# Kernel tuning notes

Hardware: AMD Instinct MI355X
Metric: run time of the kernel (lower is better)

The kernel has to match this reference:

```python
import jax, jax.numpy as jnp
import numpy as np

B, N, E, H = 16, 577, 1024, 16          # batch, tokens (1 cls + 24x24 patches), embed, heads
HD = E // H
LORA_E, LORA_R = 4, 16                   # LoRA experts, rank
AD_E, AD_D = 4, 64                       # adapter experts, bottleneck
FF = 4 * E


def setup_inputs() -> dict:
    key = jax.random.key(0)
    ks = jax.random.split(key, 12)
    p = lambda i, shape: jax.random.normal(ks[i], shape, dtype=jnp.float32) * 0.02
    return {
        "tokens": jax.random.normal(ks[0], (B, N, E), dtype=jnp.float32),
        "ln1_g": jnp.ones((E,), jnp.float32), "ln1_b": jnp.zeros((E,), jnp.float32),
        "qkv_w": p(1, (3 * E, E)), "qkv_b": jnp.zeros((3 * E,), jnp.float32),
        "proj_w": p(2, (E, E)), "proj_b": jnp.zeros((E,), jnp.float32),
        "lora_gate_w": p(3, (LORA_E, E)),
        "lora_A": p(4, (LORA_E, LORA_R, E)),
        "lora_B": p(5, (LORA_E, 3 * E, LORA_R)),
        "ln2_g": jnp.ones((E,), jnp.float32), "ln2_b": jnp.zeros((E,), jnp.float32),
        "fc1_w": p(6, (FF, E)), "fc1_b": jnp.zeros((FF,), jnp.float32),
        "fc2_w": p(7, (E, FF)), "fc2_b": jnp.zeros((E,), jnp.float32),
        "ad_gate_w": p(8, (AD_E, E)),
        "ad_down_w": p(9, (AD_E, AD_D, E)), "ad_down_b": jnp.zeros((AD_E, AD_D), jnp.float32),
        "ad_up_w": p(10, (AD_E, E, AD_D)), "ad_up_b": jnp.zeros((AD_E, E), jnp.float32),
    }


def _ln(x, g, b):
    m = x.mean(-1, keepdims=True)
    v = ((x - m) ** 2).mean(-1, keepdims=True)
    return (x - m) * jax.lax.rsqrt(v + 1e-6) * g + b


def reference(tokens, ln1_g, ln1_b, qkv_w, qkv_b, proj_w, proj_b,
              lora_gate_w, lora_A, lora_B, ln2_g, ln2_b,
              fc1_w, fc1_b, fc2_w, fc2_b,
              ad_gate_w, ad_down_w, ad_down_b, ad_up_w, ad_up_b):
    # ---- attention with MoE-LoRA delta on fused QKV ----
    normed = _ln(tokens, ln1_g, ln1_b)                      # [B,N,E]
    qkv = normed @ qkv_w.T + qkv_b                          # [B,N,3E]
    gates = jax.nn.softmax(normed @ lora_gate_w.T, axis=-1)  # [B,N,X]
    h = jnp.einsum('bnd,xrd->bnxr', normed, lora_A)         # low-rank down
    delta = jnp.einsum('bnxr,bnx,xor->bno', h, gates, lora_B)  # gate-weighted up
    qkv = (qkv + delta).reshape(B, N, 3, H, HD).transpose(2, 0, 3, 1, 4)
    q, k, v = qkv[0], qkv[1], qkv[2]                        # [B,H,N,hd]
    scores = jnp.einsum('bhqd,bhkd->bhqk', q, k) * (HD ** -0.5)
    probs = jax.nn.softmax(scores, axis=-1)
    ctx = jnp.einsum('bhqk,bhkd->bhqd', probs, v)
    ctx = ctx.transpose(0, 2, 1, 3).reshape(B, N, E)
    tokens = tokens + (ctx @ proj_w.T + proj_b)
    # ---- MLP + MoE adapter branch (shared norm2 input) ----
    mlp_in = _ln(tokens, ln2_g, ln2_b)
    mlp_out = jax.nn.gelu(mlp_in @ fc1_w.T + fc1_b, approximate=False) @ fc2_w.T + fc2_b
    ag = jax.nn.softmax(mlp_in @ ad_gate_w.T, axis=-1)       # [B,N,Xa]
    ah = jax.nn.gelu(jnp.einsum('bnd,xhd->bnxh', mlp_in, ad_down_w) + ad_down_b,
                     approximate=False)
    ad_out = (jnp.einsum('bnxh,bnx,xoh->bno', ah, ag, ad_up_w)
              + jnp.einsum('bnx,xo->bno', ag, ad_up_b))
    return tokens + mlp_out + ad_out
```

## Files before the change

### kernel.cpp

```cpp
#include <hip/hip_runtime.h>
#include <math.h>

#define TOK 9232
#define EMB 1024
#define NQKV 3072
#define FFD 4096
#define NSEQ 577

typedef __bf16 bf16x8 __attribute__((ext_vector_type(8)));
typedef float f32x4 __attribute__((ext_vector_type(4)));
typedef unsigned short ushort8 __attribute__((ext_vector_type(8)));
typedef unsigned short ushort4v __attribute__((ext_vector_type(4)));

typedef __attribute__((address_space(3))) unsigned int lds_u32_t;
typedef const __attribute__((address_space(1))) unsigned int glob_u32_t;

__device__ __forceinline__ void async16(void* lds, const void* g) {
    __builtin_amdgcn_global_load_lds((glob_u32_t*)g, (lds_u32_t*)lds, 16, 0, 0);
}

__device__ __forceinline__ unsigned short f2bf(float f) {
    unsigned int u = __builtin_bit_cast(unsigned int, f);
    u = (u + 0x7fffu + ((u >> 16) & 1u)) >> 16;
    return (unsigned short)u;
}
__device__ __forceinline__ float bf2f(unsigned short s) {
    unsigned int u = ((unsigned int)s) << 16;
    return __builtin_bit_cast(float, u);
}
__device__ __forceinline__ float gelu_exact(float x) {
    return 0.5f * x * (1.0f + erff(x * 0.70710678118654752f));
}

__global__ void k_pack_all(const float* __restrict__ s_qkv, const float* __restrict__ s_proj,
                           const float* __restrict__ s_fc1, const float* __restrict__ s_fc2,
                           const float* __restrict__ s_la,  const float* __restrict__ s_ad,
                           unsigned short* __restrict__ d_qkv, unsigned short* __restrict__ d_proj,
                           unsigned short* __restrict__ d_fc1, unsigned short* __restrict__ d_fc2,
                           unsigned short* __restrict__ d_la,  unsigned short* __restrict__ d_ad) {
    int stride = gridDim.x * 256;
    for (int i4 = blockIdx.x * 256 + threadIdx.x; i4 < 3227648; i4 += stride) {
        const float* s; unsigned short* d; int local;
        if (i4 < 786432)       { s = s_qkv;  d = d_qkv;  local = i4; }
        else if (i4 < 1048576) { s = s_proj; d = d_proj; local = i4 - 786432; }
        else if (i4 < 2097152) { s = s_fc1;  d = d_fc1;  local = i4 - 1048576; }
        else if (i4 < 3145728) { s = s_fc2;  d = d_fc2;  local = i4 - 2097152; }
        else if (i4 < 3162112) { s = s_la;   d = d_la;   local = i4 - 3145728; }
        else                   { s = s_ad;   d = d_ad;   local = i4 - 3162112; }
        float4 v = ((const float4*)s)[local];
        ushort4v o;
        o[0] = f2bf(v.x); o[1] = f2bf(v.y); o[2] = f2bf(v.z); o[3] = f2bf(v.w);
        ((ushort4v*)d)[local] = o;
    }
}
__global__ void k_pack_bcat(const float* __restrict__ Bw, unsigned short* __restrict__ out) {
    int i = blockIdx.x * 256 + threadIdx.x;
    if (i >= 3072 * 64) return;
    int o = i >> 6, j = i & 63, x = j >> 4, r = j & 15;
    out[o * 64 + j] = f2bf(Bw[x * 3072 * 16 + o * 16 + r]);
}
__global__ void k_pack_u(const float* __restrict__ Uw, unsigned short* __restrict__ out) {
    int i = blockIdx.x * 256 + threadIdx.x;
    if (i >= 1024 * 256) return;
    int o = i >> 8, j = i & 255, x = j >> 6, h = j & 63;
    out[o * 256 + j] = f2bf(Uw[x * 65536 + o * 64 + h]);
}

__global__ __launch_bounds__(256) void k_ln_gates(const float* __restrict__ x,
                                                  const float* __restrict__ g,
                                                  const float* __restrict__ b,
                                                  const float* __restrict__ gw,
                                                  unsigned short* __restrict__ out,
                                                  float* __restrict__ gates) {
    int t = blockIdx.x;
    int tid = threadIdx.x;
    const float* xp = x + (size_t)t * EMB;
    float4 v = ((const float4*)xp)[tid];
    float s = v.x + v.y + v.z + v.w;
    float sq = v.x * v.x + v.y * v.y + v.z * v.z + v.w * v.w;
    #pragma unroll
    for (int off = 32; off > 0; off >>= 1) {
        s += __shfl_down(s, off);
        sq += __shfl_down(sq, off);
    }
    __shared__ float red[8];
    if ((tid & 63) == 0) { red[tid >> 6] = s; red[(tid >> 6) + 4] = sq; }
    __syncthreads();
    float S = red[0] + red[1] + red[2] + red[3];
    float SQ = red[4] + red[5] + red[6] + red[7];
    float mean = S * (1.0f / EMB);
    float var = SQ * (1.0f / EMB) - mean * mean;
    float rstd = rsqrtf(var + 1e-6f);
    float4 gv = ((const float4*)g)[tid];
    float4 bv = ((const float4*)b)[tid];
    float n0 = (v.x - mean) * rstd * gv.x + bv.x;
    float n1 = (v.y - mean) * rstd * gv.y + bv.y;
    float n2 = (v.z - mean) * rstd * gv.z + bv.z;
    float n3 = (v.w - mean) * rstd * gv.w + bv.w;
    ushort4v o;
    o[0] = f2bf(n0); o[1] = f2bf(n1); o[2] = f2bf(n2); o[3] = f2bf(n3);
    ((ushort4v*)(out + (size_t)t * EMB))[tid] = o;
    float p[4];
    #pragma unroll
    for (int xx = 0; xx < 4; ++xx) {
        float4 gr = ((const float4*)(gw + xx * EMB))[tid];
        p[xx] = n0 * gr.x + n1 * gr.y + n2 * gr.z + n3 * gr.w;
    }
    #pragma unroll
    for (int off = 32; off > 0; off >>= 1) {
        #pragma unroll
        for (int xx = 0; xx < 4; ++xx) p[xx] += __shfl_down(p[xx], off);
    }
    __shared__ float red2[4][4];
    if ((tid & 63) == 0) {
        #pragma unroll
        for (int xx = 0; xx < 4; ++xx) red2[tid >> 6][xx] = p[xx];
    }
    __syncthreads();
    if (tid == 0) {
        float l[4];
        #pragma unroll
        for (int xx = 0; xx < 4; ++xx) l[xx] = red2[0][xx] + red2[1][xx] + red2[2][xx] + red2[3][xx];
        float m = fmaxf(fmaxf(l[0], l[1]), fmaxf(l[2], l[3]));
        float e[4], ssum = 0.f;
        #pragma unroll
        for (int xx = 0; xx < 4; ++xx) { e[xx] = expf(l[xx] - m); ssum += e[xx]; }
        float inv = 1.0f / ssum;
        #pragma unroll
        for (int xx = 0; xx < 4; ++xx) gates[t * 4 + xx] = e[xx] * inv;
    }
}

__global__ __launch_bounds__(256) void k_fc2init(const float* __restrict__ tok2,
                                                 const float* __restrict__ fc2b,
                                                 const float* __restrict__ ag,
                                                 const float* __restrict__ upb,
                                                 float* __restrict__ out) {
    int t = blockIdx.x;
    int tid = threadIdx.x;
    float g0 = ag[t * 4 + 0], g1 = ag[t * 4 + 1], g2 = ag[t * 4 + 2], g3 = ag[t * 4 + 3];
    float4 b0 = ((const float4*)(upb + 0 * EMB))[tid];
    float4 b1 = ((const float4*)(upb + 1 * EMB))[tid];
    float4 b2 = ((const float4*)(upb + 2 * EMB))[tid];
    float4 b3 = ((const float4*)(upb + 3 * EMB))[tid];
    float4 fb = ((const float4*)fc2b)[tid];
    float4 r = ((const float4*)(tok2 + (size_t)t * EMB))[tid];
    r.x += fb.x + g0 * b0.x + g1 * b1.x + g2 * b2.x + g3 * b3.x;
    r.y += fb.y + g0 * b0.y + g1 * b1.y + g2 * b2.y + g3 * b3.y;
    r.z += fb.z + g0 * b0.z + g1 * b1.z + g2 * b2.z + g3 * b3.z;
    r.w += fb.w + g0 * b0.w + g1 * b1.w + g2 * b2.w + g3 * b3.w;
    ((float4*)(out + (size_t)t * EMB))[tid] = r;
}

#define BAR __builtin_amdgcn_s_barrier()

template<bool GELU, bool BF16OUT, int GG, int MF, int NF>
__global__ __launch_bounds__(256) void k_gemm(
    const unsigned short* __restrict__ A, int lda,
    const unsigned short* __restrict__ W, int ldw, int K1,
    int M, int N,
    const unsigned short* __restrict__ A2, const unsigned short* __restrict__ W2, int K2,
    const float* __restrict__ bias, const float* __restrict__ resid,
    const float* __restrict__ aux,
    void* __restrict__ Cout, int ldc, int gy)
{
    constexpr int CA = MF * 4;
    constexpr int CB = NF * 4;
    constexpr int CT = CA + CB;
    constexpr int CPW = CT / 4;
    constexpr int BUFB = CT * 1024;
    __shared__ __attribute__((aligned(16))) char Sbuf[2 * BUFB];

    int tid = threadIdx.x;
    int nwg = gridDim.x, orig = blockIdx.x;
    int xcd = orig & 7, lid = orig >> 3;
    int q = nwg >> 3, r = nwg & 7;
    int wg = (xcd < r ? xcd * (q + 1) : r * (q + 1) + (xcd - r) * q) + lid;
    int bm = (wg / gy) * (MF * 32);
    int bn = (wg % gy) * (NF * 32);

    int l = tid & 63, w = tid >> 6;
    int wr = w >> 1, wc = w & 1;
    int lr = l & 15;
    int sslot = (((l & 7) ^ (l >> 3)) << 3);

    int KT1 = K1 >> 6, KT2 = K2 >> 6;
    int KT = KT1 + KT2;

    const unsigned short* A2s = A2 ? A2 : A;
    const unsigned short* W2s = W2 ? W2 : W;
    int K2s = A2 ? K2 : lda;

    const unsigned short* sp1[CPW];
    const unsigned short* sp2[CPW];
    int ldsu[CPW];
    #pragma unroll
    for (int j = 0; j < CPW; ++j) {
        int c = w * CPW + j;
        ldsu[j] = c << 10;
        if (c < CA) {
            int rw = bm + c * 8 + (l >> 3); if (rw > M - 1) rw = M - 1;
            sp1[j] = A + (size_t)rw * lda + sslot;
            sp2[j] = A2s + (size_t)rw * K2s + sslot;
        } else {
            int rw = bn + (c - CA) * 8 + (l >> 3); if (rw > N - 1) rw = N - 1;
            sp1[j] = W + (size_t)rw * ldw + sslot;
            sp2[j] = W2s + (size_t)rw * K2s + sslot;
        }
    }

    int offA[MF][2], offB[NF][2];
    #pragma unroll
    for (int m = 0; m < MF; ++m)
        #pragma unroll
        for (int ks = 0; ks < 2; ++ks) {
            int rw = wr * (MF * 16) + m * 16 + lr;
            int g = ks * 4 + (l >> 4);
            offA[m][ks] = (rw << 7) + ((g ^ (rw & 7)) << 4);
        }
    #pragma unroll
    for (int n = 0; n < NF; ++n)
        #pragma unroll
        for (int ks = 0; ks < 2; ++ks) {
            int rw = wc * (NF * 16) + n * 16 + lr;
            int g = ks * 4 + (l >> 4);
            offB[n][ks] = (CA << 10) + (rw << 7) + ((g ^ (rw & 7)) << 4);
        }

    f32x4 acc[MF][NF];
    #pragma unroll
    for (int m = 0; m < MF; ++m)
        #pragma unroll
        for (int n = 0; n < NF; ++n) acc[m][n] = (f32x4){0.f, 0.f, 0.f, 0.f};

    auto stage = [&](int ss, int bb) {
        char* db = Sbuf + bb * BUFB;
        if (ss < KT1) {
            int ko = ss << 6;
            #pragma unroll
            for (int j = 0; j < CPW; ++j) async16(db + ldsu[j], sp1[j] + ko);
        } else {
            int ko = (ss - KT1) << 6;
            #pragma unroll
            for (int j = 0; j < CPW; ++j) async16(db + ldsu[j], sp2[j] + ko);
        }
    };

    stage(0, 0);

    #pragma unroll 1
    for (int t = 0; t < KT; ++t) {
        asm volatile("s_waitcnt vmcnt(0)" ::: "memory");
        BAR;
        __builtin_amdgcn_sched_barrier(0);
        int s = t + 1; if (s >= KT) s = 0;
        stage(s, (t + 1) & 1);
        const char* base = Sbuf + (t & 1) * BUFB;
        bf16x8 af[MF][2], bfr[NF][2];
        #pragma unroll
        for (int m = 0; m < MF; ++m)
            #pragma unroll
            for (int ks = 0; ks < 2; ++ks) af[m][ks] = *(const bf16x8*)(base + offA[m][ks]);
        #pragma unroll
        for (int n = 0; n < NF; ++n)
            #pragma unroll
            for (int ks = 0; ks < 2; ++ks) bfr[n][ks] = *(const bf16x8*)(base + offB[n][ks]);
        __builtin_amdgcn_s_setprio(1);
        #pragma unroll
        for (int m = 0; m < MF; ++m)
            #pragma unroll
            for (int n = 0; n < NF; ++n)
                #pragma unroll
                for (int ks = 0; ks < 2; ++ks)
                    acc[m][n] = __builtin_amdgcn_mfma_f32_16x16x32_bf16(af[m][ks], bfr[n][ks], acc[m][n], 0, 0, 0);
        __builtin_amdgcn_s_setprio(0);
    }

    int rbase = bm + wr * (MF * 16);
    int cbase = bn + wc * (NF * 16);
    #pragma unroll
    for (int n = 0; n < NF; ++n) {
        int col = cbase + n * 16 + lr;
        if (col >= N) continue;
        float bv = bias ? bias[col] : 0.0f;
        #pragma unroll
        for (int m = 0; m < MF; ++m) {
            #pragma unroll
            for (int rr = 0; rr < 4; ++rr) {
                int row = rbase + m * 16 + (l >> 4) * 4 + rr;
                if (row >= M) continue;
                float c = acc[m][n][rr] + bv;
                if (GELU) c = gelu_exact(c);
                if (GG > 0) c *= aux[row * 4 + col / (GG > 0 ? GG : 1)];
                if (resid) c += resid[(size_t)row * ldc + col];
                if (BF16OUT) ((unsigned short*)Cout)[(size_t)row * ldc + col] = f2bf(c);
                else ((float*)Cout)[(size_t)row * ldc + col] = c;
            }
        }
    }
}

__global__ __launch_bounds__(256) void k_attn(const unsigned short* __restrict__ qkv,
                                              unsigned short* __restrict__ ctx) {
    int bh = blockIdx.x;
    int qt = blockIdx.y;
    int b = bh >> 4, h = bh & 15;
    int tid = threadIdx.x;
    int l = tid & 63;
    int w = tid >> 6;
    int lr = l & 15;
    int lk = (l >> 4) * 8;

    __shared__ unsigned short Qs[64][72];
    __shared__ unsigned short Ks[64][72];
    __shared__ unsigned short Vt[64][72];
    __shared__ unsigned short Ps[64][72];

    const size_t base = (size_t)b * NSEQ * NQKV + (size_t)h * 64;
    int q0 = qt * 64;

    {
        int row = tid >> 2, ds = (tid & 3) * 16;
        int qrow = q0 + row;
        if (qrow < NSEQ) {
            const unsigned short* src = qkv + base + (size_t)qrow * NQKV + ds;
            #pragma unroll
            for (int j = 0; j < 16; ++j) Qs[row][ds + j] = f2bf(bf2f(src[j]) * 0.125f);
        } else {
            #pragma unroll
            for (int j = 0; j < 16; ++j) Qs[row][ds + j] = 0;
        }
    }

    float m_run[4], l_run[4];
    f32x4 o[4];
    #pragma unroll
    for (int r = 0; r < 4; ++r) { m_run[r] = -1e30f; l_run[r] = 0.0f; }
    #pragma unroll
    for (int n = 0; n < 4; ++n) o[n] = (f32x4){0.f, 0.f, 0.f, 0.f};

    for (int kt = 0; kt < 10; ++kt) {
        __syncthreads();
        {
            int row = tid >> 2, ds = (tid & 3) * 16;
            int key = kt * 64 + row;
            if (key < NSEQ) {
                const unsigned short* ksrc = qkv + base + (size_t)key * NQKV + 1024 + ds;
                *(ushort8*)&Ks[row][ds] = *(const ushort8*)ksrc;
                *(ushort8*)&Ks[row][ds + 8] = *(const ushort8*)(ksrc + 8);
                const unsigned short* vsrc = qkv + base + (size_t)key * NQKV + 2048 + ds;
                #pragma unroll
                for (int j = 0; j < 16; ++j) Vt[ds + j][row] = vsrc[j];
            } else {
                ushort8 z = {};
                *(ushort8*)&Ks[row][ds] = z;
                *(ushort8*)&Ks[row][ds + 8] = z;
                #pragma unroll
                for (int j = 0; j < 16; ++j) Vt[ds + j][row] = 0;
            }
        }
        __syncthreads();

        f32x4 s[4];
        #pragma unroll
        for (int n = 0; n < 4; ++n) s[n] = (f32x4){0.f, 0.f, 0.f, 0.f};
        #pragma unroll
        for (int ks = 0; ks < 2; ++ks) {
            bf16x8 qa = *(const bf16x8*)&Qs[w * 16 + lr][ks * 32 + lk];
            #pragma unroll
            for (int n = 0; n < 4; ++n) {
                bf16x8 kb = *(const bf16x8*)&Ks[n * 16 + lr][ks * 32 + lk];
                s[n] = __builtin_amdgcn_mfma_f32_16x16x32_bf16(qa, kb, s[n], 0, 0, 0);
            }
        }
        #pragma unroll
        for (int n = 0; n < 4; ++n) {
            int col = kt * 64 + n * 16 + lr;
            if (col >= NSEQ) {
                #pragma unroll
                for (int r = 0; r < 4; ++r) s[n][r] = -1e30f;
            }
        }
        float tmax[4];
        #pragma unroll
        for (int r = 0; r < 4; ++r)
            tmax[r] = fmaxf(fmaxf(s[0][r], s[1][r]), fmaxf(s[2][r], s[3][r]));
        #pragma unroll
        for (int off = 1; off < 16; off <<= 1) {
            #pragma unroll
            for (int r = 0; r < 4; ++r) tmax[r] = fmaxf(tmax[r], __shfl_xor(tmax[r], off));
        }
        float alpha[4], rs[4];
        #pragma unroll
        for (int r = 0; r < 4; ++r) {
            float mn = fmaxf(m_run[r], tmax[r]);
            alpha[r] = __expf(m_run[r] - mn);
            m_run[r] = mn;
            rs[r] = 0.0f;
        }
        #pragma unroll
        for (int n = 0; n < 4; ++n) {
            #pragma unroll
            for (int r = 0; r < 4; ++r) {
                float p = __expf(s[n][r] - m_run[r]);
                s[n][r] = p;
                rs[r] += p;
            }
        }
        #pragma unroll
        for (int off = 1; off < 16; off <<= 1) {
            #pragma unroll
            for (int r = 0; r < 4; ++r) rs[r] += __shfl_xor(rs[r], off);
        }
        #pragma unroll
        for (int r = 0; r < 4; ++r) l_run[r] = l_run[r] * alpha[r] + rs[r];
        #pragma unroll
        for (int n = 0; n < 4; ++n) {
            #pragma unroll
            for (int r = 0; r < 4; ++r) o[n][r] *= alpha[r];
        }
        #pragma unroll
        for (int n = 0; n < 4; ++n) {
            #pragma unroll
            for (int r = 0; r < 4; ++r)
                Ps[w * 16 + (l >> 4) * 4 + r][n * 16 + lr] = f2bf(s[n][r]);
        }
        __syncthreads();
        #pragma unroll
        for (int ks = 0; ks < 2; ++ks) {
            bf16x8 pa = *(const bf16x8*)&Ps[w * 16 + lr][ks * 32 + lk];
            #pragma unroll
            for (int n = 0; n < 4; ++n) {
                bf16x8 vb = *(const bf16x8*)&Vt[n * 16 + lr][ks * 32 + lk];
                o[n] = __builtin_amdgcn_mfma_f32_16x16x32_bf16(pa, vb, o[n], 0, 0, 0);
            }
        }
    }
    #pragma unroll
    for (int r = 0; r < 4; ++r) {
        int qrow = q0 + w * 16 + (l >> 4) * 4 + r;
        if (qrow < NSEQ) {
            float inv = (l_run[r] > 0.f) ? 1.0f / l_run[r] : 0.0f;
            #pragma unroll
            for (int n = 0; n < 4; ++n)
                ctx[((size_t)b * NSEQ + qrow) * EMB + h * 64 + n * 16 + lr] = f2bf(o[n][r] * inv);
        }
    }
}

extern "C" void kernel_launch(void* const* d_in, const int* in_sizes, int n_in,
                              void* d_out, int out_size, void* d_ws, size_t ws_size,
                              hipStream_t stream) {
    const float* tokens      = (const float*)d_in[0];
    const float* ln1_g       = (const float*)d_in[1];
    const float* ln1_b       = (const float*)d_in[2];
    const float* qkv_w       = (const float*)d_in[3];
    const float* qkv_b       = (const float*)d_in[4];
    const float* proj_w      = (const float*)d_in[5];
    const float* proj_b      = (const float*)d_in[6];
    const float* lora_gate_w = (const float*)d_in[7];
    const float* lora_A      = (const float*)d_in[8];
    const float* lora_B      = (const float*)d_in[9];
    const float* ln2_g       = (const float*)d_in[10];
    const float* ln2_b       = (const float*)d_in[11];
    const float* fc1_w       = (const float*)d_in[12];
    const float* fc1_b       = (const float*)d_in[13];
    const float* fc2_w       = (const float*)d_in[14];
    const float* fc2_b       = (const float*)d_in[15];
    const float* ad_gate_w   = (const float*)d_in[16];
    const float* ad_down_w   = (const float*)d_in[17];
    const float* ad_down_b   = (const float*)d_in[18];
    const float* ad_up_w     = (const float*)d_in[19];
    const float* ad_up_b     = (const float*)d_in[20];

    char* ws = (char*)d_ws;
    size_t off = 0;
    auto alloc = [&](size_t bytes) -> void* {
        void* p = ws + off;
        off += (bytes + 255) & ~(size_t)255;
        return p;
    };

    unsigned short* w_qkv  = (unsigned short*)alloc((size_t)NQKV * EMB * 2);
    unsigned short* w_proj = (unsigned short*)alloc((size_t)EMB * EMB * 2);
    unsigned short* w_fc1  = (unsigned short*)alloc((size_t)FFD * EMB * 2);
    unsigned short* w_fc2  = (unsigned short*)alloc((size_t)EMB * FFD * 2);
    unsigned short* w_acat = (unsigned short*)alloc((size_t)64 * EMB * 2);
    unsigned short* w_bcat = (unsigned short*)alloc((size_t)NQKV * 64 * 2);
    unsigned short* w_dcat = (unsigned short*)alloc((size_t)256 * EMB * 2);
    unsigned short* w_u    = (unsigned short*)alloc((size_t)EMB * 256 * 2);

    unsigned short* u1 = (unsigned short*)alloc((size_t)TOK * EMB * 2);
    unsigned short* u2 = (unsigned short*)alloc((size_t)TOK * EMB * 2);
    unsigned short* u3 = (unsigned short*)alloc((size_t)TOK * FFD * 2);
    float* tok2  = (float*)alloc((size_t)TOK * EMB * 4);
    unsigned short* hw  = (unsigned short*)alloc((size_t)TOK * 64 * 2);
    unsigned short* ahw = (unsigned short*)alloc((size_t)TOK * 256 * 2);
    float* gates = (float*)alloc((size_t)TOK * 4 * 4);
    float* ag    = (float*)alloc((size_t)TOK * 4 * 4);

    unsigned short* normed = u1;
    unsigned short* mlpin  = u1;
    unsigned short* ctx    = u2;
    unsigned short* qkv    = u3;
    unsigned short* h1     = u3;

    k_pack_all<<<2048, 256, 0, stream>>>(qkv_w, proj_w, fc1_w, fc2_w, lora_A, ad_down_w,
                                         w_qkv, w_proj, w_fc1, w_fc2, w_acat, w_dcat);
    k_pack_bcat<<<(NQKV * 64 + 255) / 256, 256, 0, stream>>>(lora_B, w_bcat);
    k_pack_u<<<(EMB * 256 + 255) / 256, 256, 0, stream>>>(ad_up_w, w_u);

    k_ln_gates<<<TOK, 256, 0, stream>>>(tokens, ln1_g, ln1_b, lora_gate_w, normed, gates);
    k_gemm<false, true, 16, 2, 2><<<145, 256, 0, stream>>>(
        normed, EMB, w_acat, EMB, EMB, TOK, 64,
        nullptr, nullptr, 0, nullptr, nullptr, gates, hw, 64, 1);
    k_gemm<false, true, 0, 4, 2><<<73 * 48, 256, 0, stream>>>(
        normed, EMB, w_qkv, EMB, EMB, TOK, NQKV,
        hw, w_bcat, 64, qkv_b, nullptr, nullptr, qkv, NQKV, 48);
    k_attn<<<dim3(256, 10), 256, 0, stream>>>(qkv, ctx);
    k_gemm<false, false, 0, 2, 2><<<145 * 16, 256, 0, stream>>>(
        ctx, EMB, w_proj, EMB, EMB, TOK, EMB,
        nullptr, nullptr, 0, proj_b, tokens, nullptr, tok2, EMB, 16);
    k_ln_gates<<<TOK, 256, 0, stream>>>(tok2, ln2_g, ln2_b, ad_gate_w, mlpin, ag);
    k_gemm<true, true, 64, 2, 2><<<145 * 4, 256, 0, stream>>>(
        mlpin, EMB, w_dcat, EMB, EMB, TOK, 256,
        nullptr, nullptr, 0, ad_down_b, nullptr, ag, ahw, 256, 4);
    k_fc2init<<<TOK, 256, 0, stream>>>(tok2, fc2_b, ag, ad_up_b, (float*)d_out);
    k_gemm<true, true, 0, 4, 2><<<73 * 64, 256, 0, stream>>>(
        mlpin, EMB, w_fc1, EMB, EMB, TOK, FFD,
        nullptr, nullptr, 0, fc1_b, nullptr, nullptr, h1, FFD, 64);
    k_gemm<false, false, 0, 4, 2><<<73 * 16, 256, 0, stream>>>(
        h1, FFD, w_fc2, FFD, FFD, TOK, EMB,
        ahw, w_u, 256, nullptr, (const float*)d_out, nullptr, (float*)d_out, EMB, 16);
}
```

Before: 669.8 us.

## Triple-buffer GEMM K-loop and remap workgroups into column-grouped tile order

Moves the GEMM main loop from double to triple LDS buffering, prefetching two K-steps ahead with a partial vmcnt wait instead of draining all loads. This is meant to hide global-to-LDS latency better. It also remaps workgroup IDs so groups of CN adjacent N-tiles sweep all M-tiles together, which should improve weight reuse in L2. The cost is 1.5x LDS per block, which may lower occupancy. The vmcnt counts assume a fixed number of loads per stage.

```diff
diff --git a/kernel.cpp b/kernel.cpp
--- a/kernel.cpp
+++ b/kernel.cpp
@@ -154,7 +154,7 @@
 
 #define BAR __builtin_amdgcn_s_barrier()
 
-template<bool GELU, bool BF16OUT, int GG, int MF, int NF>
+template<bool GELU, bool BF16OUT, int GG, int MF, int NF, int CN>
 __global__ __launch_bounds__(256) void k_gemm(
     const unsigned short* __restrict__ A, int lda,
     const unsigned short* __restrict__ W, int ldw, int K1,
@@ -169,15 +169,20 @@
     constexpr int CT = CA + CB;
     constexpr int CPW = CT / 4;
     constexpr int BUFB = CT * 1024;
-    __shared__ __attribute__((aligned(16))) char Sbuf[2 * BUFB];
+    __shared__ __attribute__((aligned(16))) char Sbuf[3 * BUFB];
 
     int tid = threadIdx.x;
     int nwg = gridDim.x, orig = blockIdx.x;
     int xcd = orig & 7, lid = orig >> 3;
     int q = nwg >> 3, r = nwg & 7;
     int wg = (xcd < r ? xcd * (q + 1) : r * (q + 1) + (xcd - r) * q) + lid;
-    int bm = (wg / gy) * (MF * 32);
-    int bn = (wg % gy) * (NF * 32);
+    int nmt = nwg / gy;
+    int ni = wg % CN;
+    int tmp = wg / CN;
+    int mt = tmp % nmt;
+    int nt = (tmp / nmt) * CN + ni;
+    int bm = mt * (MF * 32);
+    int bn = nt * (NF * 32);
 
     int l = tid & 63, w = tid >> 6;
     int wr = w >> 1, wc = w & 1;
@@ -247,15 +252,18 @@
     };
 
     stage(0, 0);
-
+    stage(1, 1);
+
+    int cb = 0, sb = 2;
     #pragma unroll 1
     for (int t = 0; t < KT; ++t) {
-        asm volatile("s_waitcnt vmcnt(0)" ::: "memory");
+        if constexpr (CPW == 6) asm volatile("s_waitcnt vmcnt(6)" ::: "memory");
+        else                    asm volatile("s_waitcnt vmcnt(4)" ::: "memory");
         BAR;
         __builtin_amdgcn_sched_barrier(0);
-        int s = t + 1; if (s >= KT) s = 0;
-        stage(s, (t + 1) & 1);
-        const char* base = Sbuf + (t & 1) * BUFB;
+        int s = t + 2; if (s >= KT) s -= KT;
+        stage(s, sb);
+        const char* base = Sbuf + cb * BUFB;
         bf16x8 af[MF][2], bfr[NF][2];
         #pragma unroll
         for (int m = 0; m < MF; ++m)
@@ -274,6 +282,8 @@
                 for (int ks = 0; ks < 2; ++ks)
                     acc[m][n] = __builtin_amdgcn_mfma_f32_16x16x32_bf16(af[m][ks], bfr[n][ks], acc[m][n], 0, 0, 0);
         __builtin_amdgcn_s_setprio(0);
+        cb = (cb == 2) ? 0 : cb + 1;
+        sb = (sb == 2) ? 0 : sb + 1;
     }
 
     int rbase = bm + wr * (MF * 16);
@@ -511,25 +521,25 @@
     k_pack_u<<<(EMB * 256 + 255) / 256, 256, 0, stream>>>(ad_up_w, w_u);
 
     k_ln_gates<<<TOK, 256, 0, stream>>>(tokens, ln1_g, ln1_b, lora_gate_w, normed, gates);
-    k_gemm<false, true, 16, 2, 2><<<145, 256, 0, stream>>>(
+    k_gemm<false, true, 16, 2, 2, 1><<<145, 256, 0, stream>>>(
         normed, EMB, w_acat, EMB, EMB, TOK, 64,
         nullptr, nullptr, 0, nullptr, nullptr, gates, hw, 64, 1);
-    k_gemm<false, true, 0, 4, 2><<<73 * 48, 256, 0, stream>>>(
+    k_gemm<false, true, 0, 4, 2, 8><<<73 * 48, 256, 0, stream>>>(
         normed, EMB, w_qkv, EMB, EMB, TOK, NQKV,
         hw, w_bcat, 64, qkv_b, nullptr, nullptr, qkv, NQKV, 48);
     k_attn<<<dim3(256, 10), 256, 0, stream>>>(qkv, ctx);
-    k_gemm<false, false, 0, 2, 2><<<145 * 16, 256, 0, stream>>>(
+    k_gemm<false, false, 0, 2, 2, 8><<<145 * 16, 256, 0, stream>>>(
         ctx, EMB, w_proj, EMB, EMB, TOK, EMB,
         nullptr, nullptr, 0, proj_b, tokens, nullptr, tok2, EMB, 16);
     k_ln_gates<<<TOK, 256, 0, stream>>>(tok2, ln2_g, ln2_b, ad_gate_w, mlpin, ag);
-    k_gemm<true, true, 64, 2, 2><<<145 * 4, 256, 0, stream>>>(
+    k_gemm<true, true, 64, 2, 2, 4><<<145 * 4, 256, 0, stream>>>(
         mlpin, EMB, w_dcat, EMB, EMB, TOK, 256,
         nullptr, nullptr, 0, ad_down_b, nullptr, ag, ahw, 256, 4);
     k_fc2init<<<TOK, 256, 0, stream>>>(tok2, fc2_b, ag, ad_up_b, (float*)d_out);
-    k_gemm<true, true, 0, 4, 2><<<73 * 64, 256, 0, stream>>>(
+    k_gemm<true, true, 0, 4, 2, 8><<<73 * 64, 256, 0, stream>>>(
         mlpin, EMB, w_fc1, EMB, EMB, TOK, FFD,
         nullptr, nullptr, 0, fc1_b, nullptr, nullptr, h1, FFD, 64);
-    k_gemm<false, false, 0, 4, 2><<<73 * 16, 256, 0, stream>>>(
+    k_gemm<false, false, 0, 4, 2, 8><<<73 * 16, 256, 0, stream>>>(
         h1, FFD, w_fc2, FFD, FFD, TOK, EMB,
         ahw, w_u, 256, nullptr, (const float*)d_out, nullptr, (float*)d_out, EMB, 16);
 }
```

New measurement: 719.6 us. +7.4%, slower.
